# Kernel tuning notes

Measured on AMD Instinct MI355X. Metric: run time of the kernel, lower is better.

The kernel has to match this reference:

```python
import jax, jax.numpy as jnp
import numpy as np

COST_CLASS = 1.0
COST_BBOX = 5.0
COST_GIOU = 2.0
BS, Q, NUM_CLASSES, T = 16, 900, 92, 256  # T targets per image


def box_cxcywh_to_xyxy(x):
    cx, cy, w, h = x[..., 0], x[..., 1], x[..., 2], x[..., 3]
    return jnp.stack([cx - 0.5 * w, cy - 0.5 * h, cx + 0.5 * w, cy + 0.5 * h], axis=-1)


def generalized_box_iou(b1, b2):
    # b1: [N,4], b2: [M,4] xyxy -> [N,M]
    area1 = (b1[:, 2] - b1[:, 0]) * (b1[:, 3] - b1[:, 1])
    area2 = (b2[:, 2] - b2[:, 0]) * (b2[:, 3] - b2[:, 1])
    lt = jnp.maximum(b1[:, None, :2], b2[None, :, :2])
    rb = jnp.minimum(b1[:, None, 2:], b2[None, :, 2:])
    wh = jnp.clip(rb - lt, 0.0)
    inter = wh[..., 0] * wh[..., 1]
    union = area1[:, None] + area2[None, :] - inter
    iou = inter / union
    lt_e = jnp.minimum(b1[:, None, :2], b2[None, :, :2])
    rb_e = jnp.maximum(b1[:, None, 2:], b2[None, :, 2:])
    wh_e = jnp.clip(rb_e - lt_e, 0.0)
    area = wh_e[..., 0] * wh_e[..., 1]
    return iou - (area - union) / area


def lsa(cost):
    """Jonker-Volgenant style linear sum assignment (minimize). Returns (row_ind, col_ind)
    sorted by row, matching scipy.optimize.linear_sum_assignment semantics for rectangular C."""
    cost = np.asarray(cost, dtype=np.float64)
    transposed = cost.shape[0] > cost.shape[1]
    if transposed:
        cost = cost.T
    n, m = cost.shape  # n <= m
    INF = np.inf
    u = np.zeros(n + 1)
    v = np.zeros(m + 1)
    p = np.zeros(m + 1, dtype=np.int64)  # p[j]: 1-indexed row assigned to col j (0 = free)
    for i in range(1, n + 1):
        p[0] = i
        j0 = 0
        minv = np.full(m + 1, INF)
        way = np.zeros(m + 1, dtype=np.int64)
        used = np.zeros(m + 1, dtype=bool)
        while True:
            used[j0] = True
            i0 = p[j0]
            cur = np.concatenate(([INF], cost[i0 - 1, :] - u[i0] - v[1:]))
            free = ~used
            free[0] = False
            upd = free & (cur < minv)
            minv = np.where(upd, cur, minv)
            way = np.where(upd, j0, way)
            mfree = np.where(free, minv, INF)
            j1 = int(np.argmin(mfree))
            delta = mfree[j1]
            u[p[used]] += delta
            v[used] -= delta
            minv[~used] -= delta
            j0 = j1
            if p[j0] == 0:
                break
        while j0 != 0:
            j1 = way[j0]
            p[j0] = p[j1]
            j0 = j1
    rows = p[1:] - 1
    cols = np.arange(m)
    mask = rows >= 0
    r, c = rows[mask], cols[mask]
    if transposed:
        r, c = c, r
    order = np.argsort(r, kind='stable')
    return r[order], c[order]


def setup_inputs() -> dict:
    key = jax.random.key(0)
    k1, k2, k3, k4 = jax.random.split(key, 4)
    return {
        'pred_logits': jax.random.normal(k1, (BS, Q, NUM_CLASSES), dtype=jnp.float32),
        'pred_boxes': jax.random.uniform(k2, (BS, Q, 4), dtype=jnp.float32),
        'tgt_labels': jax.random.randint(k3, (BS * T,), 0, NUM_CLASSES, dtype=jnp.int64),
        'tgt_bbox': jax.random.uniform(k4, (BS * T, 4), dtype=jnp.float32),
    }


def reference(pred_logits, pred_boxes, tgt_labels, tgt_bbox):
    bs, nq, nc = pred_logits.shape
    out_prob = jax.nn.softmax(pred_logits.reshape(bs * nq, nc), axis=-1)
    out_bbox = pred_boxes.reshape(bs * nq, 4)
    cost_class = -out_prob[:, tgt_labels]                                  # [bs*Q, sumT]
    cost_bbox = jnp.abs(out_bbox[:, None, :] - tgt_bbox[None, :, :]).sum(-1)  # L1 cdist
    cost_giou = -generalized_box_iou(box_cxcywh_to_xyxy(out_bbox), box_cxcywh_to_xyxy(tgt_bbox))
    C = COST_BBOX * cost_bbox + COST_CLASS * cost_class + COST_GIOU * cost_giou
    C = C.reshape(bs, nq, -1)
    t = tgt_bbox.shape[0] // bs
    Cnp = np.asarray(C)
    rows, cols = [], []
    for b in range(bs):  # per-image assignment (mirrors scipy dispatch in the original)
        r, c = lsa(Cnp[b, :, b * t:(b + 1) * t])
        rows.append(r)
        cols.append(c)
    return C, jnp.asarray(np.stack(rows), dtype=jnp.int64), jnp.asarray(np.stack(cols), dtype=jnp.int64)
```

## Files before the change

### kernel.cpp

```cpp
#include <hip/hip_runtime.h>
#include <math.h>
#include <limits.h>

#define BSZ 16
#define NQ  900
#define NCL 92
#define NT  256
#define SUMT (BSZ*NT)
#define MM  NQ
#define NN  NT
#define NSLOT 15
#define QCHUNK 60
#define WAVES 16
#define BLKT (WAVES*64)
#define RING 512
#define ARR_CAP 4000

__global__ __launch_bounds__(256) void prob_kernel(
    const float* __restrict__ logits, float* __restrict__ P) {
#pragma clang fp contract(off)
  const int w = threadIdx.x >> 6, lane = threadIdx.x & 63;
  const int r = blockIdx.x * 4 + w;
  const size_t base = (size_t)r * NCL;
  const float x1 = logits[base + lane];
  const float x2 = (lane + 64 < NCL) ? logits[base + lane + 64] : -INFINITY;
  float m = fmaxf(x1, x2);
  #pragma unroll
  for (int k = 1; k < 64; k <<= 1) m = fmaxf(m, __shfl_xor(m, k));
  const float e1 = expf(x1 - m);
  const float e2 = (lane + 64 < NCL) ? expf(x2 - m) : 0.f;
  float ssum = e1 + e2;
  #pragma unroll
  for (int k = 1; k < 64; k <<= 1) ssum += __shfl_xor(ssum, k);
  P[base + lane] = e1 / ssum;
  if (lane + 64 < NCL) P[base + lane + 64] = e2 / ssum;
}

__global__ __launch_bounds__(256) void cost_kernel2(
    const float* __restrict__ P, const float* __restrict__ boxes,
    const int* __restrict__ labels, const float* __restrict__ tbox,
    float* __restrict__ C, float* __restrict__ costT,
    unsigned long long* __restrict__ upack) {
#pragma clang fp contract(off)
  const int tid = threadIdx.x;
  const int jt = blockIdx.x * 256 + tid;
  const int b  = blockIdx.z;
  const int q0 = blockIdx.y * QCHUNK;
  const bool diag = (blockIdx.x == b) && (costT != nullptr);

  __shared__ float sP[QCHUNK * NCL];
  __shared__ float sB[QCHUNK * 4];

  const size_t pbase = (size_t)(b * NQ + q0) * NCL;
  for (int x = tid; x < QCHUNK * NCL; x += 256) sP[x] = P[pbase + x];
  const size_t bbase = (size_t)(b * NQ + q0) * 4;
  if (tid < QCHUNK * 4) sB[tid] = boxes[bbase + tid];

  const float4 tb = ((const float4*)tbox)[jt];
  const int lab = labels[jt];
  const float tx1 = tb.x - 0.5f*tb.z, ty1 = tb.y - 0.5f*tb.w;
  const float tx2 = tb.x + 0.5f*tb.z, ty2 = tb.y + 0.5f*tb.w;
  const float area2 = (tx2 - tx1) * (ty2 - ty1);
  __syncthreads();

  float* tr = diag ? (costT + ((size_t)(b * NT + tid)) * MM + q0) : nullptr;
  unsigned long long best = ~0ull;

  for (int qq = 0; qq < QCHUNK; ++qq) {
    const float cx = sB[qq*4+0], cy = sB[qq*4+1];
    const float w  = sB[qq*4+2], h  = sB[qq*4+3];
    const float cc = -sP[qq*NCL + lab];
    const float bx1 = cx - 0.5f*w, by1 = cy - 0.5f*h;
    const float bx2 = cx + 0.5f*w, by2 = cy + 0.5f*h;
    const float area1 = (bx2 - bx1) * (by2 - by1);
    const float d0 = fabsf(cx - tb.x), d1 = fabsf(cy - tb.y);
    const float d2 = fabsf(w - tb.z),  d3 = fabsf(h - tb.w);
    const float cb = ((d0 + d1) + d2) + d3;
    const float ltx = fmaxf(bx1, tx1), lty = fmaxf(by1, ty1);
    const float rbx = fminf(bx2, tx2), rby = fminf(by2, ty2);
    const float iw = fmaxf(rbx - ltx, 0.f), ih = fmaxf(rby - lty, 0.f);
    const float inter = iw * ih;
    const float uni = (area1 + area2) - inter;
    const float iou = inter / uni;
    const float ex1 = fminf(bx1, tx1), ey1 = fminf(by1, ty1);
    const float ex2 = fmaxf(bx2, tx2), ey2 = fmaxf(by2, ty2);
    const float ew = fmaxf(ex2 - ex1, 0.f), eh = fmaxf(ey2 - ey1, 0.f);
    const float ea = ew * eh;
    const float giou = iou - (ea - uni) / ea;
    const float cval = (5.0f*cb + 1.0f*cc) + 2.0f*(-giou);
    C[(size_t)(b*NQ + q0 + qq) * SUMT + jt] = cval;
    if (diag) {
      tr[qq] = cval;
      unsigned bts = __float_as_uint(cval);
      bts = (bts & 0x80000000u) ? ~bts : (bts | 0x80000000u);
      const unsigned long long pk =
          ((unsigned long long)bts << 32) | (unsigned)(q0 + qq);
      if (pk < best) best = pk;
    }
  }
  if (diag && upack) atomicMin(&upack[b * NN + tid], best);
}

__global__ __launch_bounds__(256) void cost_kernel_fb(
    const float* __restrict__ logits, const float* __restrict__ boxes,
    const int* __restrict__ labels, const float* __restrict__ tbox,
    float* __restrict__ C, float* __restrict__ costT) {
#pragma clang fp contract(off)
  const int bq  = blockIdx.x;
  const int b   = bq / NQ;
  const int tid = threadIdx.x;
  __shared__ float lg[NCL];
  __shared__ float red[128];
  if (tid < NCL) lg[tid] = logits[(size_t)bq * NCL + tid];
  __syncthreads();
  if (tid < 128) red[tid] = (tid < NCL) ? lg[tid] : -INFINITY;
  __syncthreads();
  for (int s = 64; s > 0; s >>= 1) { if (tid < s) red[tid] = fmaxf(red[tid], red[tid+s]); __syncthreads(); }
  const float mx = red[0];
  __syncthreads();
  float e = 0.f;
  if (tid < NCL) e = expf(lg[tid] - mx);
  if (tid < 128) red[tid] = e;
  __syncthreads();
  for (int s = 64; s > 0; s >>= 1) { if (tid < s) red[tid] += red[tid+s]; __syncthreads(); }
  const float sm = red[0];
  __syncthreads();
  if (tid < NCL) lg[tid] = e / sm;
  __syncthreads();
  const float cx = boxes[(size_t)bq*4+0], cy = boxes[(size_t)bq*4+1];
  const float w  = boxes[(size_t)bq*4+2], h  = boxes[(size_t)bq*4+3];
  const float bx1 = cx - 0.5f*w, by1 = cy - 0.5f*h;
  const float bx2 = cx + 0.5f*w, by2 = cy + 0.5f*h;
  const float area1 = (bx2 - bx1) * (by2 - by1);
  const int q = bq - b * NQ;
  for (int jt = tid; jt < SUMT; jt += 256) {
    const float4 tb = ((const float4*)tbox)[jt];
    const int lab = labels[jt];
    const float cc = -lg[lab];
    const float d0 = fabsf(cx - tb.x), d1 = fabsf(cy - tb.y);
    const float d2 = fabsf(w - tb.z),  d3 = fabsf(h - tb.w);
    const float cb = ((d0 + d1) + d2) + d3;
    const float tx1 = tb.x - 0.5f*tb.z, ty1 = tb.y - 0.5f*tb.w;
    const float tx2 = tb.x + 0.5f*tb.z, ty2 = tb.y + 0.5f*tb.w;
    const float area2 = (tx2 - tx1) * (ty2 - ty1);
    const float ltx = fmaxf(bx1, tx1), lty = fmaxf(by1, ty1);
    const float rbx = fminf(bx2, tx2), rby = fminf(by2, ty2);
    const float iw = fmaxf(rbx - ltx, 0.f), ih = fmaxf(rby - lty, 0.f);
    const float inter = iw * ih;
    const float uni = (area1 + area2) - inter;
    const float iou = inter / uni;
    const float ex1 = fminf(bx1, tx1), ey1 = fminf(by1, ty1);
    const float ex2 = fmaxf(bx2, tx2), ey2 = fmaxf(by2, ty2);
    const float ew = fmaxf(ex2 - ex1, 0.f), eh = fmaxf(ey2 - ey1, 0.f);
    const float ea = ew * eh;
    const float giou = iou - (ea - uni) / ea;
    const float cval = (5.0f*cb + 1.0f*cc) + 2.0f*(-giou);
    C[(size_t)bq * SUMT + jt] = cval;
    if (costT && (jt >> 8) == b) costT[(size_t)jt * MM + q] = cval;
  }
}

__global__ __launch_bounds__(BLKT) void lsa_kernel(
    const float* __restrict__ C, const float* __restrict__ costT,
    const unsigned long long* __restrict__ upack,
    float* __restrict__ rows_out, float* __restrict__ cols_out) {
  const int b   = blockIdx.x;
  const int tid = threadIdx.x;

  __shared__ double u[NN + 1];
  __shared__ int    p[MM + 1];
  __shared__ int    wayl[MM + 1];
  __shared__ int    claim[MM + 1];
  __shared__ int    rowargmin[NN];
  __shared__ unsigned char rowass[NN];
  __shared__ int    listj[MM + 1];
  __shared__ double listD[MM + 1];
  __shared__ double vs[MM + 1];
  __shared__ int    qring[RING];
  __shared__ int    qhead_sh, qtail_sh, steps_sh;
  __shared__ int    bid_i[WAVES], bid_j[WAVES];
  __shared__ double bid_b1[WAVES], bid_b2[WAVES];

  for (int j = tid; j <= MM; j += BLKT) { p[j] = 0; claim[j] = INT_MAX; vs[j] = 0.0; }
  if (upack) {
    if (tid < NN) {
      const unsigned long long pk = upack[b * NN + tid];
      const unsigned key = (unsigned)(pk >> 32);
      const unsigned bts = (key & 0x80000000u) ? (key & 0x7fffffffu) : ~key;
      u[tid + 1] = (double)__uint_as_float(bts);
      rowargmin[tid] = (int)(pk & 0xffffffffu);
    }
  } else if (costT || C) {
    if (tid < NN) {
      const float* rowptr = C + ((size_t)(b * NQ)) * SUMT + b * NT + tid;
      float mn = INFINITY; int am = 0;
      #pragma unroll 4
      for (int q = 0; q < NQ; ++q) {
        const float cv = rowptr[(size_t)q * SUMT];
        if (cv < mn) { mn = cv; am = q; }
      }
      u[tid + 1] = (double)mn;
      rowargmin[tid] = am;
    }
  }
  if (tid == 0) u[0] = 0.0;
  __syncthreads();
  if (tid < NN) atomicMin(&claim[rowargmin[tid] + 1], tid + 1);
  __syncthreads();
  if (tid < NN) {
    const int am = rowargmin[tid];
    const bool got = (claim[am + 1] == tid + 1);
    rowass[tid] = got ? 1 : 0;
    if (got) p[am + 1] = tid + 1;
  }
  __syncthreads();

  const int lane = tid & 63;
  const int wv   = tid >> 6;
  const float* slab = costT ? costT + (size_t)b * NT * MM : nullptr;

  if (tid < 64) {
    int fcnt = 0;
    #pragma unroll
    for (int c = 0; c < 4; ++c) {
      const bool fr = !rowass[c * 64 + tid];
      const unsigned long long mk = __ballot(fr);
      const int rk = __popcll(mk & ((1ull << tid) - 1ull));
      if (fr) qring[fcnt + rk] = c * 64 + tid + 1;
      fcnt += __popcll(mk);
    }
    if (tid == 0) { qhead_sh = 0; qtail_sh = fcnt; steps_sh = 0; }
  }
  __syncthreads();

  if (slab) {
    while (true) {
      const int head = qhead_sh, tail = qtail_sh, st = steps_sh;
      if (head >= tail || st >= ARR_CAP) break;
      const int nact = ((tail - head) < WAVES) ? (tail - head) : WAVES;

      if (wv < nact) {
        const int i = qring[(head + wv) & (RING - 1)];
        const float* rowp = slab + (size_t)(i - 1) * MM;
        double b1 = INFINITY, b2 = INFINITY; int j1 = MM + 2;
        #pragma unroll
        for (int s = 0; s < NSLOT; ++s) {
          const int j = s * 64 + lane + 1;
          if (j <= MM) {
            const double cand = (double)rowp[j - 1] - vs[j];
            if (cand < b1) { b2 = b1; b1 = cand; j1 = j; }
            else           { b2 = fmin(b2, cand); }
          }
        }
        #pragma unroll
        for (int m = 1; m < 64; m <<= 1) {
          const double ob1 = __shfl_xor(b1, m);
          const double ob2 = __shfl_xor(b2, m);
          const int    oj1 = __shfl_xor(j1, m);
          if (ob1 < b1 || (ob1 == b1 && oj1 < j1)) {
            b2 = fmin(b1, ob2); b1 = ob1; j1 = oj1;
          } else {
            b2 = fmin(b2, ob1);
          }
        }
        if (lane == 0) { bid_i[wv] = i; bid_j[wv] = j1; bid_b1[wv] = b1; bid_b2[wv] = b2; }
      }
      __syncthreads();

      if (tid < nact) {
        const int j1 = bid_j[tid];
        bool dup = false;
        for (int e = 0; e < tid; ++e) if (bid_j[e] == j1) dup = true;
        if (dup) {
          const int slot = atomicAdd(&qtail_sh, 1);
          qring[slot & (RING - 1)] = bid_i[tid];
        } else {
          const double amt = bid_b2[tid] - bid_b1[tid];
          vs[j1] -= amt;
          u[bid_i[tid]] = bid_b2[tid];
          const int k = p[j1];
          p[j1] = bid_i[tid];
          rowass[bid_i[tid] - 1] = 1;
          if (k) {
            rowass[k - 1] = 0;
            const int slot = atomicAdd(&qtail_sh, 1);
            qring[slot & (RING - 1)] = k;
          }
        }
      }
      if (tid == 0) { qhead_sh += nact; steps_sh += nact; }
      __syncthreads();
    }
  }

  if (tid >= 64) return;

  double v_r[NSLOT];
  #pragma unroll
  for (int s = 0; s < NSLOT; ++s) {
    const int j = s * 64 + lane + 1;
    v_r[s] = (j <= MM) ? vs[j] : 0.0;
  }

  for (int ii = 1; ii <= NN; ++ii) {
    if (rowass[ii - 1]) continue;

    double M_r[NSLOT];
    #pragma unroll
    for (int s = 0; s < NSLOT; ++s) M_r[s] = INFINITY;
    unsigned int used = (lane < 4) ? 0u : (1u << 14);
    int    lcount = 0;
    int    j0 = 0;
    double Dsel = 0.0;
    double D = 0.0;
    bool   okrow = true;

    while (true) {
      const int    i0 = (j0 == 0) ? ii : p[j0];
      const double us = u[i0] - Dsel;
      const float* rowp = slab ? slab + (size_t)(i0 - 1) * MM : nullptr;

      double best = INFINITY; int bestj = MM + 2;
      #pragma unroll
      for (int s = 0; s < NSLOT; ++s) {
        if (!(used & (1u << s))) {
          const int j = s * 64 + lane + 1;
          const float cf = rowp ? rowp[j - 1]
              : C[((size_t)(b*NQ + (j-1)))*SUMT + (b*NT + i0 - 1)];
          const double cand = ((double)cf - v_r[s]) - us;
          if (cand < M_r[s]) { M_r[s] = cand; wayl[j] = j0; }
          if (M_r[s] < best) { best = M_r[s]; bestj = j; }
        }
      }
      #pragma unroll
      for (int m = 1; m < 64; m <<= 1) {
        const double ov = __shfl_xor(best, m);
        const int    oj = __shfl_xor(bestj, m);
        if (ov < best || (ov == best && oj < bestj)) { best = ov; bestj = oj; }
      }
      const int j1 = bestj;
      if (j1 > MM) { okrow = false; break; }
      D = best;
      if (lane == ((j1 - 1) & 63)) used |= 1u << ((j1 - 1) >> 6);
      if (p[j1] == 0) { j0 = j1; break; }
      if (lane == 0) { listj[lcount] = j1; listD[lcount] = D; }
      lcount++;
      j0 = j1; Dsel = D;
    }

    if (okrow) {
      for (int e = 0; e < lcount; ++e) {
        const int    je = listj[e];
        const double amt = D - listD[e];
        if (lane == ((je - 1) & 63)) v_r[(je - 1) >> 6] -= amt;
        if (lane == 0) u[p[je]] += amt;
      }
      if (lane == 0) {
        u[ii] += D;
        int jj = j0;
        while (jj) { const int jn = wayl[jj]; const int pn = (jn == 0) ? ii : p[jn]; p[jj] = pn; jj = jn; }
        rowass[ii - 1] = 1;
      }
    }
  }

  int base = 0;
  #pragma unroll
  for (int s = 0; s < NSLOT; ++s) {
    const int j = s * 64 + lane + 1;
    const bool a = (j <= MM) && (p[j] > 0);
    const unsigned long long mask = __ballot(a);
    const int rank = __popcll(mask & ((1ull << lane) - 1ull));
    if (a) {
      rows_out[b*NT + base + rank] = (float)(j - 1);
      cols_out[b*NT + base + rank] = (float)(p[j] - 1);
    }
    base += __popcll(mask);
  }
}

extern "C" void kernel_launch(void* const* d_in, const int* in_sizes, int n_in,
                              void* d_out, int out_size, void* d_ws, size_t ws_size,
                              hipStream_t stream) {
  const float* logits = (const float*)d_in[0];
  const float* boxes  = (const float*)d_in[1];
  const int*   labels = (const int*)d_in[2];
  const float* tbox   = (const float*)d_in[3];

  float* C    = (float*)d_out;
  float* rows = C + (size_t)BSZ * NQ * SUMT;
  float* cols = rows + (size_t)BSZ * NT;

  const size_t needT = (size_t)SUMT * MM * sizeof(float);
  const size_t needP = (size_t)BSZ * NQ * NCL * sizeof(float);
  const size_t needU = (size_t)BSZ * NN * sizeof(unsigned long long);

  if (ws_size >= needP + needT + needU) {
    float* P     = (float*)d_ws;
    float* costT = P + (size_t)BSZ * NQ * NCL;
    unsigned long long* upack = (unsigned long long*)(costT + (size_t)SUMT * MM);
    hipMemsetAsync(upack, 0xFF, needU, stream);
    hipLaunchKernelGGL(prob_kernel, dim3(BSZ*NQ/4), dim3(256), 0, stream, logits, P);
    hipLaunchKernelGGL(cost_kernel2, dim3(SUMT/256, NQ/QCHUNK, BSZ), dim3(256), 0, stream,
                       P, boxes, labels, tbox, C, costT, upack);
    hipLaunchKernelGGL(lsa_kernel, dim3(BSZ), dim3(BLKT), 0, stream,
                       C, costT, upack, rows, cols);
  } else if (ws_size >= needP + needT) {
    float* P     = (float*)d_ws;
    float* costT = P + (size_t)BSZ * NQ * NCL;
    hipLaunchKernelGGL(prob_kernel, dim3(BSZ*NQ/4), dim3(256), 0, stream, logits, P);
    hipLaunchKernelGGL(cost_kernel2, dim3(SUMT/256, NQ/QCHUNK, BSZ), dim3(256), 0, stream,
                       P, boxes, labels, tbox, C, costT, (unsigned long long*)nullptr);
    hipLaunchKernelGGL(lsa_kernel, dim3(BSZ), dim3(BLKT), 0, stream,
                       C, costT, (const unsigned long long*)nullptr, rows, cols);
  } else if (ws_size >= needT) {
    float* costT = (float*)d_ws;
    hipLaunchKernelGGL(cost_kernel_fb, dim3(BSZ*NQ), dim3(256), 0, stream,
                       logits, boxes, labels, tbox, C, costT);
    hipLaunchKernelGGL(lsa_kernel, dim3(BSZ), dim3(BLKT), 0, stream,
                       C, costT, (const unsigned long long*)nullptr, rows, cols);
  } else {
    hipLaunchKernelGGL(cost_kernel_fb, dim3(BSZ*NQ), dim3(256), 0, stream,
                       logits, boxes, labels, tbox, C, (float*)nullptr);
    hipLaunchKernelGGL(lsa_kernel, dim3(BSZ), dim3(BLKT), 0, stream,
                       C, (float*)nullptr, (const unsigned long long*)nullptr, rows, cols);
  }
}
```

Baseline: 388.7 us.

## Fuse softmax into cost kernel and double auction bids per round

The separate softmax kernel and its probability buffer in workspace are removed. Each cost block now loads raw logits into shared memory and normalises its 60 query rows in place before computing costs. This saves a launch and a global round trip, at the price of redoing the softmax in every target-column block (16x redundant). In the auction phase of the assignment kernel, each round now processes up to 32 bids instead of 16, with each wave handling two rows, to halve the number of synchronised rounds. The trade-off is more duplicate-column conflicts per round.

```diff
diff --git a/kernel.cpp b/kernel.cpp
--- a/kernel.cpp
+++ b/kernel.cpp
@@ -13,31 +13,12 @@
 #define QCHUNK 60
 #define WAVES 16
 #define BLKT (WAVES*64)
+#define BIDS (2*WAVES)
 #define RING 512
 #define ARR_CAP 4000
 
-__global__ __launch_bounds__(256) void prob_kernel(
-    const float* __restrict__ logits, float* __restrict__ P) {
-#pragma clang fp contract(off)
-  const int w = threadIdx.x >> 6, lane = threadIdx.x & 63;
-  const int r = blockIdx.x * 4 + w;
-  const size_t base = (size_t)r * NCL;
-  const float x1 = logits[base + lane];
-  const float x2 = (lane + 64 < NCL) ? logits[base + lane + 64] : -INFINITY;
-  float m = fmaxf(x1, x2);
-  #pragma unroll
-  for (int k = 1; k < 64; k <<= 1) m = fmaxf(m, __shfl_xor(m, k));
-  const float e1 = expf(x1 - m);
-  const float e2 = (lane + 64 < NCL) ? expf(x2 - m) : 0.f;
-  float ssum = e1 + e2;
-  #pragma unroll
-  for (int k = 1; k < 64; k <<= 1) ssum += __shfl_xor(ssum, k);
-  P[base + lane] = e1 / ssum;
-  if (lane + 64 < NCL) P[base + lane + 64] = e2 / ssum;
-}
-
 __global__ __launch_bounds__(256) void cost_kernel2(
-    const float* __restrict__ P, const float* __restrict__ boxes,
+    const float* __restrict__ logits, const float* __restrict__ boxes,
     const int* __restrict__ labels, const float* __restrict__ tbox,
     float* __restrict__ C, float* __restrict__ costT,
     unsigned long long* __restrict__ upack) {
@@ -52,16 +33,35 @@
   __shared__ float sB[QCHUNK * 4];
 
   const size_t pbase = (size_t)(b * NQ + q0) * NCL;
-  for (int x = tid; x < QCHUNK * NCL; x += 256) sP[x] = P[pbase + x];
+  for (int x = tid; x < QCHUNK * NCL; x += 256) sP[x] = logits[pbase + x];
   const size_t bbase = (size_t)(b * NQ + q0) * 4;
   if (tid < QCHUNK * 4) sB[tid] = boxes[bbase + tid];
+  __syncthreads();
+
+  {
+    const int w = tid >> 6, lane = tid & 63;
+    for (int r = w; r < QCHUNK; r += 4) {
+      const float x1 = sP[r * NCL + lane];
+      const float x2 = (lane + 64 < NCL) ? sP[r * NCL + lane + 64] : -INFINITY;
+      float m = fmaxf(x1, x2);
+      #pragma unroll
+      for (int k = 1; k < 64; k <<= 1) m = fmaxf(m, __shfl_xor(m, k));
+      const float e1 = expf(x1 - m);
+      const float e2 = (lane + 64 < NCL) ? expf(x2 - m) : 0.f;
+      float ssum = e1 + e2;
+      #pragma unroll
+      for (int k = 1; k < 64; k <<= 1) ssum += __shfl_xor(ssum, k);
+      sP[r * NCL + lane] = e1 / ssum;
+      if (lane + 64 < NCL) sP[r * NCL + lane + 64] = e2 / ssum;
+    }
+  }
+  __syncthreads();
 
   const float4 tb = ((const float4*)tbox)[jt];
   const int lab = labels[jt];
   const float tx1 = tb.x - 0.5f*tb.z, ty1 = tb.y - 0.5f*tb.w;
   const float tx2 = tb.x + 0.5f*tb.z, ty2 = tb.y + 0.5f*tb.w;
   const float area2 = (tx2 - tx1) * (ty2 - ty1);
-  __syncthreads();
 
   float* tr = diag ? (costT + ((size_t)(b * NT + tid)) * MM + q0) : nullptr;
   unsigned long long best = ~0ull;
@@ -101,65 +101,6 @@
   if (diag && upack) atomicMin(&upack[b * NN + tid], best);
 }
 
-__global__ __launch_bounds__(256) void cost_kernel_fb(
-    const float* __restrict__ logits, const float* __restrict__ boxes,
-    const int* __restrict__ labels, const float* __restrict__ tbox,
-    float* __restrict__ C, float* __restrict__ costT) {
-#pragma clang fp contract(off)
-  const int bq  = blockIdx.x;
-  const int b   = bq / NQ;
-  const int tid = threadIdx.x;
-  __shared__ float lg[NCL];
-  __shared__ float red[128];
-  if (tid < NCL) lg[tid] = logits[(size_t)bq * NCL + tid];
-  __syncthreads();
-  if (tid < 128) red[tid] = (tid < NCL) ? lg[tid] : -INFINITY;
-  __syncthreads();
-  for (int s = 64; s > 0; s >>= 1) { if (tid < s) red[tid] = fmaxf(red[tid], red[tid+s]); __syncthreads(); }
-  const float mx = red[0];
-  __syncthreads();
-  float e = 0.f;
-  if (tid < NCL) e = expf(lg[tid] - mx);
-  if (tid < 128) red[tid] = e;
-  __syncthreads();
-  for (int s = 64; s > 0; s >>= 1) { if (tid < s) red[tid] += red[tid+s]; __syncthreads(); }
-  const float sm = red[0];
-  __syncthreads();
-  if (tid < NCL) lg[tid] = e / sm;
-  __syncthreads();
-  const float cx = boxes[(size_t)bq*4+0], cy = boxes[(size_t)bq*4+1];
-  const float w  = boxes[(size_t)bq*4+2], h  = boxes[(size_t)bq*4+3];
-  const float bx1 = cx - 0.5f*w, by1 = cy - 0.5f*h;
-  const float bx2 = cx + 0.5f*w, by2 = cy + 0.5f*h;
-  const float area1 = (bx2 - bx1) * (by2 - by1);
-  const int q = bq - b * NQ;
-  for (int jt = tid; jt < SUMT; jt += 256) {
-    const float4 tb = ((const float4*)tbox)[jt];
-    const int lab = labels[jt];
-    const float cc = -lg[lab];
-    const float d0 = fabsf(cx - tb.x), d1 = fabsf(cy - tb.y);
-    const float d2 = fabsf(w - tb.z),  d3 = fabsf(h - tb.w);
-    const float cb = ((d0 + d1) + d2) + d3;
-    const float tx1 = tb.x - 0.5f*tb.z, ty1 = tb.y - 0.5f*tb.w;
-    const float tx2 = tb.x + 0.5f*tb.z, ty2 = tb.y + 0.5f*tb.w;
-    const float area2 = (tx2 - tx1) * (ty2 - ty1);
-    const float ltx = fmaxf(bx1, tx1), lty = fmaxf(by1, ty1);
-    const float rbx = fminf(bx2, tx2), rby = fminf(by2, ty2);
-    const float iw = fmaxf(rbx - ltx, 0.f), ih = fmaxf(rby - lty, 0.f);
-    const float inter = iw * ih;
-    const float uni = (area1 + area2) - inter;
-    const float iou = inter / uni;
-    const float ex1 = fminf(bx1, tx1), ey1 = fminf(by1, ty1);
-    const float ex2 = fmaxf(bx2, tx2), ey2 = fmaxf(by2, ty2);
-    const float ew = fmaxf(ex2 - ex1, 0.f), eh = fmaxf(ey2 - ey1, 0.f);
-    const float ea = ew * eh;
-    const float giou = iou - (ea - uni) / ea;
-    const float cval = (5.0f*cb + 1.0f*cc) + 2.0f*(-giou);
-    C[(size_t)bq * SUMT + jt] = cval;
-    if (costT && (jt >> 8) == b) costT[(size_t)jt * MM + q] = cval;
-  }
-}
-
 __global__ __launch_bounds__(BLKT) void lsa_kernel(
     const float* __restrict__ C, const float* __restrict__ costT,
     const unsigned long long* __restrict__ upack,
@@ -178,8 +119,8 @@
   __shared__ double vs[MM + 1];
   __shared__ int    qring[RING];
   __shared__ int    qhead_sh, qtail_sh, steps_sh;
-  __shared__ int    bid_i[WAVES], bid_j[WAVES];
-  __shared__ double bid_b1[WAVES], bid_b2[WAVES];
+  __shared__ int    bid_i[BIDS], bid_j[BIDS];
+  __shared__ double bid_b1[BIDS], bid_b2[BIDS];
 
   for (int j = tid; j <= MM; j += BLKT) { p[j] = 0; claim[j] = INT_MAX; vs[j] = 0.0; }
   if (upack) {
@@ -190,7 +131,7 @@
       u[tid + 1] = (double)__uint_as_float(bts);
       rowargmin[tid] = (int)(pk & 0xffffffffu);
     }
-  } else if (costT || C) {
+  } else {
     if (tid < NN) {
       const float* rowptr = C + ((size_t)(b * NQ)) * SUMT + b * NT + tid;
       float mn = INFINITY; int am = 0;
@@ -237,37 +178,41 @@
     while (true) {
       const int head = qhead_sh, tail = qtail_sh, st = steps_sh;
       if (head >= tail || st >= ARR_CAP) break;
-      const int nact = ((tail - head) < WAVES) ? (tail - head) : WAVES;
-
-      if (wv < nact) {
-        const int i = qring[(head + wv) & (RING - 1)];
-        const float* rowp = slab + (size_t)(i - 1) * MM;
-        double b1 = INFINITY, b2 = INFINITY; int j1 = MM + 2;
-        #pragma unroll
-        for (int s = 0; s < NSLOT; ++s) {
-          const int j = s * 64 + lane + 1;
-          if (j <= MM) {
-            const double cand = (double)rowp[j - 1] - vs[j];
-            if (cand < b1) { b2 = b1; b1 = cand; j1 = j; }
-            else           { b2 = fmin(b2, cand); }
+      int navail = tail - head; if (navail > BIDS) navail = BIDS;
+
+      #pragma unroll
+      for (int rep = 0; rep < 2; ++rep) {
+        const int slot = rep * WAVES + wv;
+        if (slot < navail) {
+          const int i = qring[(head + slot) & (RING - 1)];
+          const float* rowp = slab + (size_t)(i - 1) * MM;
+          double b1 = INFINITY, b2 = INFINITY; int j1 = MM + 2;
+          #pragma unroll
+          for (int s = 0; s < NSLOT; ++s) {
+            const int j = s * 64 + lane + 1;
+            if (j <= MM) {
+              const double cand = (double)rowp[j - 1] - vs[j];
+              if (cand < b1) { b2 = b1; b1 = cand; j1 = j; }
+              else           { b2 = fmin(b2, cand); }
+            }
           }
+          #pragma unroll
+          for (int m = 1; m < 64; m <<= 1) {
+            const double ob1 = __shfl_xor(b1, m);
+            const double ob2 = __shfl_xor(b2, m);
+            const int    oj1 = __shfl_xor(j1, m);
+            if (ob1 < b1 || (ob1 == b1 && oj1 < j1)) {
+              b2 = fmin(b1, ob2); b1 = ob1; j1 = oj1;
+            } else {
+              b2 = fmin(b2, ob1);
+            }
+          }
+          if (lane == 0) { bid_i[slot] = i; bid_j[slot] = j1; bid_b1[slot] = b1; bid_b2[slot] = b2; }
         }
-        #pragma unroll
-        for (int m = 1; m < 64; m <<= 1) {
-          const double ob1 = __shfl_xor(b1, m);
-          const double ob2 = __shfl_xor(b2, m);
-          const int    oj1 = __shfl_xor(j1, m);
-          if (ob1 < b1 || (ob1 == b1 && oj1 < j1)) {
-            b2 = fmin(b1, ob2); b1 = ob1; j1 = oj1;
-          } else {
-            b2 = fmin(b2, ob1);
-          }
-        }
-        if (lane == 0) { bid_i[wv] = i; bid_j[wv] = j1; bid_b1[wv] = b1; bid_b2[wv] = b2; }
       }
       __syncthreads();
 
-      if (tid < nact) {
+      if (tid < navail) {
         const int j1 = bid_j[tid];
         bool dup = false;
         for (int e = 0; e < tid; ++e) if (bid_j[e] == j1) dup = true;
@@ -288,7 +233,7 @@
           }
         }
       }
-      if (tid == 0) { qhead_sh += nact; steps_sh += nact; }
+      if (tid == 0) { qhead_sh += navail; steps_sh += navail; }
       __syncthreads();
     }
   }
@@ -392,36 +337,26 @@
   float* cols = rows + (size_t)BSZ * NT;
 
   const size_t needT = (size_t)SUMT * MM * sizeof(float);
-  const size_t needP = (size_t)BSZ * NQ * NCL * sizeof(float);
   const size_t needU = (size_t)BSZ * NN * sizeof(unsigned long long);
 
-  if (ws_size >= needP + needT + needU) {
-    float* P     = (float*)d_ws;
-    float* costT = P + (size_t)BSZ * NQ * NCL;
+  if (ws_size >= needT + needU) {
+    float* costT = (float*)d_ws;
     unsigned long long* upack = (unsigned long long*)(costT + (size_t)SUMT * MM);
     hipMemsetAsync(upack, 0xFF, needU, stream);
-    hipLaunchKernelGGL(prob_kernel, dim3(BSZ*NQ/4), dim3(256), 0, stream, logits, P);
     hipLaunchKernelGGL(cost_kernel2, dim3(SUMT/256, NQ/QCHUNK, BSZ), dim3(256), 0, stream,
-                       P, boxes, labels, tbox, C, costT, upack);
+                       logits, boxes, labels, tbox, C, costT, upack);
     hipLaunchKernelGGL(lsa_kernel, dim3(BSZ), dim3(BLKT), 0, stream,
                        C, costT, upack, rows, cols);
-  } else if (ws_size >= needP + needT) {
-    float* P     = (float*)d_ws;
-    float* costT = P + (size_t)BSZ * NQ * NCL;
-    hipLaunchKernelGGL(prob_kernel, dim3(BSZ*NQ/4), dim3(256), 0, stream, logits, P);
-    hipLaunchKernelGGL(cost_kernel2, dim3(SUMT/256, NQ/QCHUNK, BSZ), dim3(256), 0, stream,
-                       P, boxes, labels, tbox, C, costT, (unsigned long long*)nullptr);
-    hipLaunchKernelGGL(lsa_kernel, dim3(BSZ), dim3(BLKT), 0, stream,
-                       C, costT, (const unsigned long long*)nullptr, rows, cols);
   } else if (ws_size >= needT) {
     float* costT = (float*)d_ws;
-    hipLaunchKernelGGL(cost_kernel_fb, dim3(BSZ*NQ), dim3(256), 0, stream,
-                       logits, boxes, labels, tbox, C, costT);
+    hipLaunchKernelGGL(cost_kernel2, dim3(SUMT/256, NQ/QCHUNK, BSZ), dim3(256), 0, stream,
+                       logits, boxes, labels, tbox, C, costT, (unsigned long long*)nullptr);
     hipLaunchKernelGGL(lsa_kernel, dim3(BSZ), dim3(BLKT), 0, stream,
                        C, costT, (const unsigned long long*)nullptr, rows, cols);
   } else {
-    hipLaunchKernelGGL(cost_kernel_fb, dim3(BSZ*NQ), dim3(256), 0, stream,
-                       logits, boxes, labels, tbox, C, (float*)nullptr);
+    hipLaunchKernelGGL(cost_kernel2, dim3(SUMT/256, NQ/QCHUNK, BSZ), dim3(256), 0, stream,
+                       logits, boxes, labels, tbox, C, (float*)nullptr,
+                       (unsigned long long*)nullptr);
     hipLaunchKernelGGL(lsa_kernel, dim3(BSZ), dim3(BLKT), 0, stream,
                        C, (float*)nullptr, (const unsigned long long*)nullptr, rows, cols);
   }
```

New measurement: 411.1 us. 1.06x slower.
